# Performance work log

Measured on AMD Instinct MI355X. Metric: run time of the kernel, lower is better.

## Reference

```python
import jax, jax.numpy as jnp
import numpy as np

ATTENTION_DIM = 256
MAX_STATE_SIZE = 2000
LOCATION_FILTER = 32
LOCATION_KERNEL = 31
TEMPERATURE = 1.0
CUMULATIVE = True
MASK_VAL = -2.0 ** 32 + 1


def setup_inputs() -> dict:
    key = jax.random.key(0)
    ks = jax.random.split(key, 8)
    B, T, A, F, K = 64, 2000, ATTENTION_DIM, LOCATION_FILTER, LOCATION_KERNEL
    query = jax.random.normal(ks[0], (B, A), dtype=jnp.float32)
    prev_weights = jax.random.uniform(ks[1], (B, MAX_STATE_SIZE), dtype=jnp.float32)
    w_memory = jax.random.normal(ks[2], (B, T, A), dtype=jnp.float32)
    memory_lengths = jax.random.randint(ks[3], (B,), 1, T + 1, dtype=jnp.int32)
    conv_w = jax.random.normal(ks[4], (K, 1, F), dtype=jnp.float32) * 0.1
    conv_b = jnp.zeros((F,), dtype=jnp.float32)
    loc_w = jax.random.normal(ks[5], (F, A), dtype=jnp.float32) * 0.1
    score_v = jax.random.normal(ks[6], (A,), dtype=jnp.float32)
    score_b = jnp.zeros((A,), dtype=jnp.float32)
    return {
        "query": query,
        "prev_weights": prev_weights,
        "w_memory": w_memory,
        "memory_lengths": memory_lengths,
        "conv_w": conv_w,
        "conv_b": conv_b,
        "loc_w": loc_w,
        "score_v": score_v,
        "score_b": score_b,
    }


def reference(query, prev_weights, w_memory, memory_lengths, conv_w, conv_b, loc_w, score_v, score_b):
    B, T, A = w_memory.shape
    # location features: conv over previous alignments [B, T, 1] -> [B, T, F]
    align_prev = prev_weights[:, :T][..., None]
    f = jax.lax.conv_general_dilated(
        align_prev, conv_w, window_strides=(1,), padding="SAME",
        dimension_numbers=("NWC", "WIO", "NWC")) + conv_b
    processed_loc = jnp.einsum("btf,fa->bta", f, loc_w)  # [B, T, A]
    # Bahdanau additive score -> [B, T]
    energy = jnp.einsum(
        "a,bta->bt", score_v,
        jnp.tanh(w_memory + query[:, None, :] + processed_loc + score_b)) / TEMPERATURE
    mask = jnp.arange(T)[None, :] < memory_lengths[:, None]
    energy = jnp.where(mask, energy, MASK_VAL)
    alignments = jax.nn.softmax(energy, axis=1)
    # pad to max_state_size (static pad amount)
    output = jnp.pad(alignments, ((0, 0), (0, MAX_STATE_SIZE - T)))
    new_weights = output + prev_weights if CUMULATIVE else output
    return output, new_weights
```

## Files before the change

### kernel.cpp

```cpp
#include <hip/hip_runtime.h>
#include <cstddef>

#define B_  64
#define T_  2000
#define A_  256
#define K_  31
#define F_  32
#define TT_ 128
#define RW_ 8

typedef float v2f __attribute__((ext_vector_type(2)));

__device__ __forceinline__ float fast_tanh(float x) {
  float p = __expf(x + x);
  float r = __builtin_amdgcn_rcpf(p + 1.0f);
  return fmaf(-2.0f, r, 1.0f);
}

__device__ __forceinline__ float4 ld4(const float* p) {
  return *(const float4*)p;
}

__device__ __forceinline__ float rfl(float x) {
  return __int_as_float(__builtin_amdgcn_readfirstlane(__float_as_int(x)));
}

__global__ __launch_bounds__(256) void prep_kernel(
    const float* __restrict__ conv_w, const float* __restrict__ conv_b,
    const float* __restrict__ loc_w, const float* __restrict__ query,
    const float* __restrict__ score_b, float* __restrict__ W2,
    float* __restrict__ qb) {
  const int a = threadIdx.x;
  const int blk = blockIdx.x;
  if (blk < K_) {
    float acc = 0.f;
    #pragma unroll
    for (int f = 0; f < F_; ++f) acc = fmaf(conv_w[blk * F_ + f], loc_w[f * A_ + a], acc);
    W2[blk * A_ + a] = acc;
  } else {
    const int b = blk - K_;
    float acc = 0.f;
    #pragma unroll
    for (int f = 0; f < F_; ++f) acc = fmaf(conv_b[f], loc_w[f * A_ + a], acc);
    qb[b * A_ + a] = query[b * A_ + a] + score_b[a] + acc;
  }
}

__global__ __attribute__((amdgpu_flat_work_group_size(256, 256),
                          amdgpu_waves_per_eu(2, 4)))
void energy_kernel(
    const float* __restrict__ wmem, const float* __restrict__ pw,
    const float* __restrict__ qb, const float* __restrict__ W2,
    const float* __restrict__ score_v, float* __restrict__ energy) {
  const int b = blockIdx.y;
  const int t0 = blockIdx.x * TT_;
  const int tid = threadIdx.x;
  const int lane = tid & 63;
  const int wv = tid >> 6;

  __shared__ __align__(16) float lds_W2[K_ * A_];
  __shared__ __align__(16) float lds_pw[TT_ + 40];

  for (int idx = tid * 4; idx < K_ * A_; idx += 256 * 4)
    *(float4*)&lds_W2[idx] = ld4(W2 + idx);

  if (tid < TT_ + 40) {
    const int g = t0 - 15 + tid;
    lds_pw[tid] = (g >= 0 && g < T_) ? pw[b * T_ + g] : 0.f;
  }
  __syncthreads();

  const float4 qb4 = ld4(qb + b * A_ + 4 * lane);
  const float4 v4  = ld4(score_v + 4 * lane);
  const float* wrow = wmem + (size_t)b * T_ * A_ + 4 * lane;
  const float* w2l  = lds_W2 + 4 * lane;

  const int rbase = 32 * wv;

  #pragma unroll 1
  for (int i = 0; i < 32 / RW_; ++i) {
    const int widx = rbase + RW_ * i;

    float4 w4[RW_];
    #pragma unroll
    for (int j = 0; j < RW_; ++j) {
      const int t = t0 + widx + j;
      const int tc = t < T_ ? t : T_ - 1;
      w4[j] = ld4(wrow + (size_t)tc * A_);
    }

    float s[40];
    #pragma unroll
    for (int m = 0; m < 10; ++m) {
      const float4 t4 = ld4(&lds_pw[widx + 4 * m]);
      s[4 * m + 0] = rfl(t4.x); s[4 * m + 1] = rfl(t4.y);
      s[4 * m + 2] = rfl(t4.z); s[4 * m + 3] = rfl(t4.w);
    }

    v2f pl0[RW_], pl1[RW_];
    #pragma unroll
    for (int j = 0; j < RW_; ++j) { pl0[j] = (v2f)0.f; pl1[j] = (v2f)0.f; }
    #pragma unroll
    for (int k = 0; k < K_; ++k) {
      const float4 w2k = ld4(w2l + k * A_);
      const v2f wa = {w2k.x, w2k.y};
      const v2f wb = {w2k.z, w2k.w};
      #pragma unroll
      for (int j = 0; j < RW_; ++j) {
        const v2f sv = {s[j + k], s[j + k]};
        pl0[j] = __builtin_elementwise_fma(sv, wa, pl0[j]);
        pl1[j] = __builtin_elementwise_fma(sv, wb, pl1[j]);
      }
    }

    float e[RW_];
    #pragma unroll
    for (int j = 0; j < RW_; ++j) {
      const float tx = fast_tanh(w4[j].x + qb4.x + pl0[j].x);
      const float ty = fast_tanh(w4[j].y + qb4.y + pl0[j].y);
      const float tz = fast_tanh(w4[j].z + qb4.z + pl1[j].x);
      const float tw = fast_tanh(w4[j].w + qb4.w + pl1[j].y);
      e[j] = fmaf(v4.x, tx, fmaf(v4.y, ty, fmaf(v4.z, tz, v4.w * tw)));
    }

    float m0 = e[0] + __shfl_xor(e[0], 32);
    float m1 = e[1] + __shfl_xor(e[1], 32);
    float m2 = e[2] + __shfl_xor(e[2], 32);
    float m3 = e[3] + __shfl_xor(e[3], 32);
    float m4 = e[4] + __shfl_xor(e[4], 32);
    float m5 = e[5] + __shfl_xor(e[5], 32);
    float m6 = e[6] + __shfl_xor(e[6], 32);
    float m7 = e[7] + __shfl_xor(e[7], 32);
    const bool b5 = (lane & 32) != 0;
    float u0 = b5 ? m4 : m0;
    float u1 = b5 ? m5 : m1;
    float u2 = b5 ? m6 : m2;
    float u3 = b5 ? m7 : m3;
    u0 += __shfl_xor(u0, 16);
    u1 += __shfl_xor(u1, 16);
    u2 += __shfl_xor(u2, 16);
    u3 += __shfl_xor(u3, 16);
    const bool b4 = (lane & 16) != 0;
    float w0 = b4 ? u2 : u0;
    float w1 = b4 ? u3 : u1;
    w0 += __shfl_xor(w0, 8);
    w1 += __shfl_xor(w1, 8);
    float y = (lane & 8) ? w1 : w0;
    y += __shfl_xor(y, 4);
    y += __shfl_xor(y, 2);
    y += __shfl_xor(y, 1);

    const int tr = t0 + widx + (lane >> 3);
    if ((lane & 7) == 0 && tr < T_) energy[b * T_ + tr] = y;
  }
}

__global__ __launch_bounds__(256) void softmax_kernel(
    const float* __restrict__ energy, const float* __restrict__ pw,
    const int* __restrict__ lens, float* __restrict__ out) {
  const int b = blockIdx.x;
  const int tid = threadIdx.x;
  const int len = lens[b];
  __shared__ float red[4];
  const float L2E = 1.4426950408889634f;

  float mx = -3.4e38f;
  for (int t = tid; t < T_; t += 256)
    if (t < len) mx = fmaxf(mx, energy[b * T_ + t]);
  #pragma unroll
  for (int m = 1; m < 64; m <<= 1) mx = fmaxf(mx, __shfl_xor(mx, m, 64));
  if ((tid & 63) == 0) red[tid >> 6] = mx;
  __syncthreads();
  mx = fmaxf(fmaxf(red[0], red[1]), fmaxf(red[2], red[3]));
  __syncthreads();

  float sm = 0.f;
  for (int t = tid; t < T_; t += 256)
    if (t < len) sm += __builtin_amdgcn_exp2f((energy[b * T_ + t] - mx) * L2E);
  #pragma unroll
  for (int m = 1; m < 64; m <<= 1) sm += __shfl_xor(sm, m, 64);
  if ((tid & 63) == 0) red[tid >> 6] = sm;
  __syncthreads();
  sm = red[0] + red[1] + red[2] + red[3];
  const float inv = 1.0f / sm;

  for (int t = tid; t < T_; t += 256) {
    float o = 0.f;
    if (t < len)
      o = __builtin_amdgcn_exp2f((energy[b * T_ + t] - mx) * L2E) * inv;
    out[b * T_ + t] = o;
    out[B_ * T_ + b * T_ + t] = o + pw[b * T_ + t];
  }
}

extern "C" void kernel_launch(void* const* d_in, const int* in_sizes, int n_in,
                              void* d_out, int out_size, void* d_ws, size_t ws_size,
                              hipStream_t stream) {
  const float* query  = (const float*)d_in[0];
  const float* prev   = (const float*)d_in[1];
  const float* wmem   = (const float*)d_in[2];
  const int*   lens   = (const int*)d_in[3];
  const float* conv_w = (const float*)d_in[4];
  const float* conv_b = (const float*)d_in[5];
  const float* loc_w  = (const float*)d_in[6];
  const float* sv     = (const float*)d_in[7];
  const float* sb     = (const float*)d_in[8];
  float* out = (float*)d_out;
  float* ws  = (float*)d_ws;

  float* W2     = ws;
  float* qb     = ws + K_ * A_;
  float* energy = ws + K_ * A_ + B_ * A_;

  prep_kernel<<<K_ + B_, 256, 0, stream>>>(conv_w, conv_b, loc_w, query, sb, W2, qb);

  dim3 grid((T_ + TT_ - 1) / TT_, B_);
  energy_kernel<<<grid, 256, 0, stream>>>(wmem, prev, qb, W2, sv, energy);

  softmax_kernel<<<B_, 256, 0, stream>>>(energy, prev, lens, out);
}
```

Baseline: 224.5 us.

## Hold conv weights in registers and split attention dim across wave pairs

The energy kernel stops staging the 31x256 combined conv weight matrix in LDS. Each wave now owns a 128-column half of the attention dimension, with two columns per lane, and keeps its 31 weight pairs in registers. Each block covers 64 timesteps, so two waves per 32-row group each compute a partial score; the halves are combined through a small LDS buffer after a barrier. This removes per-iteration LDS reads of the weights and the 31 KB LDS footprint to allow higher occupancy, at the cost of more register pressure, twice as many blocks, and each block reloading the weights from global memory.

```diff
diff --git a/kernel.cpp b/kernel.cpp
--- a/kernel.cpp
+++ b/kernel.cpp
@@ -6,7 +6,7 @@
 #define A_  256
 #define K_  31
 #define F_  32
-#define TT_ 128
+#define TT_ 64
 #define RW_ 8
 
 typedef float v2f __attribute__((ext_vector_type(2)));
@@ -17,9 +17,8 @@
   return fmaf(-2.0f, r, 1.0f);
 }
 
-__device__ __forceinline__ float4 ld4(const float* p) {
-  return *(const float4*)p;
-}
+__device__ __forceinline__ float4 ld4(const float* p) { return *(const float4*)p; }
+__device__ __forceinline__ float2 ld2(const float* p) { return *(const float2*)p; }
 
 __device__ __forceinline__ float rfl(float x) {
   return __int_as_float(__builtin_amdgcn_readfirstlane(__float_as_int(x)));
@@ -47,7 +46,7 @@
 }
 
 __global__ __attribute__((amdgpu_flat_work_group_size(256, 256),
-                          amdgpu_waves_per_eu(2, 4)))
+                          amdgpu_waves_per_eu(4, 4)))
 void energy_kernel(
     const float* __restrict__ wmem, const float* __restrict__ pw,
     const float* __restrict__ qb, const float* __restrict__ W2,
@@ -57,12 +56,11 @@
   const int tid = threadIdx.x;
   const int lane = tid & 63;
   const int wv = tid >> 6;
-
-  __shared__ __align__(16) float lds_W2[K_ * A_];
+  const int half = wv & 1;
+  const int c0 = half * 128 + 2 * lane;
+
   __shared__ __align__(16) float lds_pw[TT_ + 40];
-
-  for (int idx = tid * 4; idx < K_ * A_; idx += 256 * 4)
-    *(float4*)&lds_W2[idx] = ld4(W2 + idx);
+  __shared__ float lds_half[2 * TT_];
 
   if (tid < TT_ + 40) {
     const int g = t0 - 15 + tid;
@@ -70,23 +68,28 @@
   }
   __syncthreads();
 
-  const float4 qb4 = ld4(qb + b * A_ + 4 * lane);
-  const float4 v4  = ld4(score_v + 4 * lane);
-  const float* wrow = wmem + (size_t)b * T_ * A_ + 4 * lane;
-  const float* w2l  = lds_W2 + 4 * lane;
-
-  const int rbase = 32 * wv;
+  v2f w2r[K_];
+  #pragma unroll
+  for (int k = 0; k < K_; ++k) {
+    const float2 w = ld2(W2 + k * A_ + c0);
+    w2r[k] = (v2f){w.x, w.y};
+  }
+  const float2 qb2 = ld2(qb + b * A_ + c0);
+  const float2 v2  = ld2(score_v + c0);
+  const float* wrow = wmem + (size_t)b * T_ * A_ + c0;
+
+  const int rbase = 32 * (wv >> 1);
 
   #pragma unroll 1
   for (int i = 0; i < 32 / RW_; ++i) {
     const int widx = rbase + RW_ * i;
 
-    float4 w4[RW_];
+    float2 w4[RW_];
     #pragma unroll
     for (int j = 0; j < RW_; ++j) {
       const int t = t0 + widx + j;
       const int tc = t < T_ ? t : T_ - 1;
-      w4[j] = ld4(wrow + (size_t)tc * A_);
+      w4[j] = ld2(wrow + (size_t)tc * A_);
     }
 
     float s[40];
@@ -97,30 +100,24 @@
       s[4 * m + 2] = rfl(t4.z); s[4 * m + 3] = rfl(t4.w);
     }
 
-    v2f pl0[RW_], pl1[RW_];
-    #pragma unroll
-    for (int j = 0; j < RW_; ++j) { pl0[j] = (v2f)0.f; pl1[j] = (v2f)0.f; }
+    v2f pl[RW_];
+    #pragma unroll
+    for (int j = 0; j < RW_; ++j) pl[j] = (v2f)0.f;
     #pragma unroll
     for (int k = 0; k < K_; ++k) {
-      const float4 w2k = ld4(w2l + k * A_);
-      const v2f wa = {w2k.x, w2k.y};
-      const v2f wb = {w2k.z, w2k.w};
       #pragma unroll
       for (int j = 0; j < RW_; ++j) {
         const v2f sv = {s[j + k], s[j + k]};
-        pl0[j] = __builtin_elementwise_fma(sv, wa, pl0[j]);
-        pl1[j] = __builtin_elementwise_fma(sv, wb, pl1[j]);
+        pl[j] = __builtin_elementwise_fma(sv, w2r[k], pl[j]);
       }
     }
 
     float e[RW_];
     #pragma unroll
     for (int j = 0; j < RW_; ++j) {
-      const float tx = fast_tanh(w4[j].x + qb4.x + pl0[j].x);
-      const float ty = fast_tanh(w4[j].y + qb4.y + pl0[j].y);
-      const float tz = fast_tanh(w4[j].z + qb4.z + pl1[j].x);
-      const float tw = fast_tanh(w4[j].w + qb4.w + pl1[j].y);
-      e[j] = fmaf(v4.x, tx, fmaf(v4.y, ty, fmaf(v4.z, tz, v4.w * tw)));
+      const float tx = fast_tanh(w4[j].x + qb2.x + pl[j].x);
+      const float ty = fast_tanh(w4[j].y + qb2.y + pl[j].y);
+      e[j] = fmaf(v2.x, tx, v2.y * ty);
     }
 
     float m0 = e[0] + __shfl_xor(e[0], 32);
@@ -150,8 +147,16 @@
     y += __shfl_xor(y, 2);
     y += __shfl_xor(y, 1);
 
-    const int tr = t0 + widx + (lane >> 3);
-    if ((lane & 7) == 0 && tr < T_) energy[b * T_ + tr] = y;
+    if ((lane & 7) == 0)
+      lds_half[half * TT_ + widx + (lane >> 3)] = y;
+  }
+
+  __syncthreads();
+
+  if (tid < TT_) {
+    const int t = t0 + tid;
+    if (t < T_)
+      energy[b * T_ + t] = lds_half[tid] + lds_half[TT_ + tid];
   }
 }
 
```

After: 216.1 us. 3.7% less time.
